# Performance work log

Hardware: AMD Instinct MI355X
Metric: run time of the kernel (lower is better)

Reference implementation:

```python
import jax, jax.numpy as jnp
import numpy as np

B, T, R = 64, 256, 256          # batch, timepoints, n_rois (T==R required by bmm path)
H, NH, DH, FF, LAT, L = 256, 8, 32, 512, 64, 2
EPS = 1e-5


def layernorm(x, g, b):
    m = x.mean(-1, keepdims=True)
    v = ((x - m) ** 2).mean(-1, keepdims=True)
    return (x - m) / jnp.sqrt(v + EPS) * g + b


def leaky_relu(x):
    return jnp.where(x >= 0, x, 0.1 * x)


def setup_inputs() -> dict:
    key = jax.random.key(0)
    ks = iter(jax.random.split(key, 64))
    def nrm(shape, s=0.02):
        return jax.random.normal(next(ks), shape, jnp.float32) * s
    return {
        "x": jax.random.normal(next(ks), (B, T, R), jnp.float32),
        "node_view": jax.random.normal(next(ks), (B, R, R), jnp.float32) * 0.1,
        "edge_view": jax.random.normal(next(ks), (B, R, R), jnp.float32) * 0.1,
        "fp_w": nrm((H, R)), "fp_b": jnp.zeros((H,)),
        "fp_g": jnp.ones((H,)), "fp_beta": jnp.zeros((H,)),
        "qkv_w": nrm((L, 3 * H, H)), "qkv_b": jnp.zeros((L, 3 * H)),
        "attn_out_w": nrm((L, H, H)), "attn_out_b": jnp.zeros((L, H)),
        "ln1_g": jnp.ones((L, H)), "ln1_b": jnp.zeros((L, H)),
        "ff1_w": nrm((L, FF, H)), "ff1_b": jnp.zeros((L, FF)),
        "ff2_w": nrm((L, H, FF)), "ff2_b": jnp.zeros((L, H)),
        "ln2_g": jnp.ones((L, H)), "ln2_b": jnp.zeros((L, H)),
        "out_w": nrm((R, H)), "out_b": jnp.zeros((R,)),
        "mu_w1": nrm((H // 2, H)), "mu_b1": jnp.zeros((H // 2,)),
        "mu_g": jnp.ones((H // 2,)), "mu_beta": jnp.zeros((H // 2,)),
        "mu_w2": nrm((LAT, H // 2)), "mu_b2": jnp.zeros((LAT,)),
        "lv_w1": nrm((H // 2, H)), "lv_b1": jnp.zeros((H // 2,)),
        "lv_g": jnp.ones((H // 2,)), "lv_beta": jnp.zeros((H // 2,)),
        "lv_w2": nrm((LAT, H // 2)), "lv_b2": jnp.zeros((LAT,)),
    }


def reference(x, node_view, edge_view, fp_w, fp_b, fp_g, fp_beta,
              qkv_w, qkv_b, attn_out_w, attn_out_b, ln1_g, ln1_b,
              ff1_w, ff1_b, ff2_w, ff2_b, ln2_g, ln2_b,
              out_w, out_b, mu_w1, mu_b1, mu_g, mu_beta, mu_w2, mu_b2,
              lv_w1, lv_b1, lv_g, lv_beta, lv_w2, lv_b2):
    # graph-view message passing: bmm(x^T, view), averaged, transposed back
    xr = jnp.swapaxes(x, 1, 2)                           # [B,R,T]
    msg = 0.5 * (jnp.einsum('brt,btq->brq', xr, node_view)
                 + jnp.einsum('brt,btq->brq', xr, edge_view))
    h = jnp.swapaxes(msg, 1, 2)                          # [B,T,R]
    # feature_proj: Linear -> LayerNorm -> LeakyReLU(0.1) -> Dropout(eval)
    h = leaky_relu(layernorm(h @ fp_w.T + fp_b, fp_g, fp_beta))  # [B,T,H]
    # TransformerEncoder (post-norm, relu FFN, dropout=identity)
    scale = 1.0 / jnp.sqrt(jnp.float32(DH))
    for i in range(L):
        qkv = h @ qkv_w[i].T + qkv_b[i]                  # [B,T,3H]
        q, k, v = jnp.split(qkv, 3, axis=-1)
        q = q.reshape(B, T, NH, DH).transpose(0, 2, 1, 3)
        k = k.reshape(B, T, NH, DH).transpose(0, 2, 1, 3)
        v = v.reshape(B, T, NH, DH).transpose(0, 2, 1, 3)
        attn = jax.nn.softmax(jnp.einsum('bhqd,bhkd->bhqk', q, k) * scale, axis=-1)
        o = jnp.einsum('bhqk,bhkd->bhqd', attn, v).transpose(0, 2, 1, 3).reshape(B, T, H)
        o = o @ attn_out_w[i].T + attn_out_b[i]
        h = layernorm(h + o, ln1_g[i], ln1_b[i])
        f = jax.nn.relu(h @ ff1_w[i].T + ff1_b[i]) @ ff2_w[i].T + ff2_b[i]
        h = layernorm(h + f, ln2_g[i], ln2_b[i])
    # fresh linear (treated as fixed params) then batched Pearson correlation
    y = h @ out_w.T + out_b                              # [B,T,R]
    data = jnp.swapaxes(y, 1, 2)                         # [B,R,T]
    c = data - data.mean(-1, keepdims=True)
    std = jnp.sqrt((c ** 2).sum(-1, keepdims=True) / (T - 1))   # unbiased, like torch.std
    cn = c / (std + 1e-8)
    corr = jnp.einsum('brt,bst->brs', cn, cn) / (T - 1)
    corr = jnp.nan_to_num(jnp.clip(corr, -1.0, 1.0), nan=0.0)   # [B,R,R]
    # heads
    pooled = h.mean(axis=1)                              # [B,H]
    mu = leaky_relu(layernorm(pooled @ mu_w1.T + mu_b1, mu_g, mu_beta)) @ mu_w2.T + mu_b2
    logvar = leaky_relu(layernorm(pooled @ lv_w1.T + lv_b1, lv_g, lv_beta)) @ lv_w2.T + lv_b2
    return mu, logvar, corr
```

## Files before the change

kernel.cpp:

```cpp
#include <hip/hip_runtime.h>
#include <hip/hip_bf16.h>
#include <math.h>

#define BB 64
#define NLAYER 2

typedef __attribute__((ext_vector_type(8))) short bfrag;
typedef __attribute__((ext_vector_type(4))) float f4_t;

__device__ __forceinline__ float dot4(float4 a, float4 b, float acc) {
    acc = fmaf(a.x, b.x, acc);
    acc = fmaf(a.y, b.y, acc);
    acc = fmaf(a.z, b.z, acc);
    acc = fmaf(a.w, b.w, acc);
    return acc;
}

__device__ __forceinline__ ushort f2bf(float f) {
    uint32_t u = __float_as_uint(f);
    uint32_t r = (u + 0x7FFFu + ((u >> 16) & 1u)) >> 16;
    return (ushort)r;
}
__device__ __forceinline__ float bf2f(ushort u) {
    return __uint_as_float(((uint32_t)u) << 16);
}

__global__ __launch_bounds__(256) void k_cvt(
    const float* __restrict__ fp_w, const float* __restrict__ qkv_w,
    const float* __restrict__ aow, const float* __restrict__ f1w,
    const float* __restrict__ f2w, const float* __restrict__ outw,
    ushort* __restrict__ dst) {
    const int g = blockIdx.x;
    const size_t idx = (size_t)g * 2048 + threadIdx.x * 8;
    const float* src;
    size_t base;
    if (g < 32)       { src = fp_w;  base = 0; }
    else if (g < 224) { src = qkv_w; base = 65536; }
    else if (g < 288) { src = aow;   base = 458752; }
    else if (g < 416) { src = f1w;   base = 589824; }
    else if (g < 544) { src = f2w;   base = 851968; }
    else              { src = outw;  base = 1114112; }
    const float4* s4 = reinterpret_cast<const float4*>(src + (idx - base));
    float4 a = s4[0], b = s4[1];
    bfrag o;
    o[0] = (short)f2bf(a.x); o[1] = (short)f2bf(a.y);
    o[2] = (short)f2bf(a.z); o[3] = (short)f2bf(a.w);
    o[4] = (short)f2bf(b.x); o[5] = (short)f2bf(b.y);
    o[6] = (short)f2bf(b.z); o[7] = (short)f2bf(b.w);
    *reinterpret_cast<bfrag*>(dst + idx) = o;
}

template <int EPI, bool WF32, bool WBF>
__global__ __launch_bounds__(256) void k_mm(
    const ushort* __restrict__ A, const ushort* __restrict__ B,
    const float* __restrict__ bias, float* __restrict__ C,
    ushort* __restrict__ Cb, int K, int N,
    size_t aStr, size_t bStr, size_t cStr) {
    __shared__ __align__(16) ushort As[128 * 72];
    __shared__ __align__(16) ushort Bs[128 * 72];
    const int tid = threadIdx.x;
    const int m0 = blockIdx.x * 128, n0 = blockIdx.y * 128;
    const size_t z = blockIdx.z;
    const int w = tid >> 6, lane = tid & 63;
    const int wm = w >> 1, wn = w & 1;
    const int fr = lane & 15, fq = lane >> 4;

    const int srow = tid >> 1, skc = (tid & 1) * 32;
    const ushort* aS = A + z * aStr + (size_t)(m0 + srow) * K + skc;
    const ushort* bS = B + z * bStr + (size_t)(n0 + srow) * K + skc;
    ushort* aD = &As[srow * 72 + skc];
    ushort* bD = &Bs[srow * 72 + skc];

    f4_t acc[4][4];
#pragma unroll
    for (int i = 0; i < 4; ++i)
#pragma unroll
        for (int j = 0; j < 4; ++j) acc[i][j] = (f4_t)0.f;

    for (int k0 = 0; k0 < K; k0 += 64) {
        {
            const bfrag* ap = reinterpret_cast<const bfrag*>(aS + k0);
            bfrag a0 = ap[0], a1 = ap[1], a2 = ap[2], a3 = ap[3];
            const bfrag* bp = reinterpret_cast<const bfrag*>(bS + k0);
            bfrag b0 = bp[0], b1 = bp[1], b2 = bp[2], b3 = bp[3];
            reinterpret_cast<bfrag*>(aD)[0] = a0;
            reinterpret_cast<bfrag*>(aD)[1] = a1;
            reinterpret_cast<bfrag*>(aD)[2] = a2;
            reinterpret_cast<bfrag*>(aD)[3] = a3;
            reinterpret_cast<bfrag*>(bD)[0] = b0;
            reinterpret_cast<bfrag*>(bD)[1] = b1;
            reinterpret_cast<bfrag*>(bD)[2] = b2;
            reinterpret_cast<bfrag*>(bD)[3] = b3;
        }
        __syncthreads();
#pragma unroll
        for (int ks = 0; ks < 2; ++ks) {
            const int kb = ks * 32 + fq * 8;
            bfrag af[4], bf[4];
#pragma unroll
            for (int fm = 0; fm < 4; ++fm)
                af[fm] = *reinterpret_cast<const bfrag*>(
                    &As[(wm * 64 + fm * 16 + fr) * 72 + kb]);
#pragma unroll
            for (int fn = 0; fn < 4; ++fn)
                bf[fn] = *reinterpret_cast<const bfrag*>(
                    &Bs[(wn * 64 + fn * 16 + fr) * 72 + kb]);
#pragma unroll
            for (int fm = 0; fm < 4; ++fm)
#pragma unroll
                for (int fn = 0; fn < 4; ++fn)
                    acc[fm][fn] = __builtin_amdgcn_mfma_f32_16x16x32_bf16(
                        bf[fn], af[fm], acc[fm][fn], 0, 0, 0);
        }
        __syncthreads();
    }

#pragma unroll
    for (int fn = 0; fn < 4; ++fn) {
        const int col0 = n0 + wn * 64 + fn * 16 + fq * 4;
        float4 bv = make_float4(0.f, 0.f, 0.f, 0.f);
        if (EPI != 3 && bias != nullptr)
            bv = *reinterpret_cast<const float4*>(&bias[col0]);
#pragma unroll
        for (int fm = 0; fm < 4; ++fm) {
            const int row = m0 + wm * 64 + fm * 16 + fr;
            float v0 = acc[fm][fn][0] + bv.x;
            float v1 = acc[fm][fn][1] + bv.y;
            float v2 = acc[fm][fn][2] + bv.z;
            float v3 = acc[fm][fn][3] + bv.w;
            if (EPI == 2) {
                v0 = fmaxf(v0, 0.f); v1 = fmaxf(v1, 0.f);
                v2 = fmaxf(v2, 0.f); v3 = fmaxf(v3, 0.f);
            }
            if (EPI == 3) {
                v0 = acc[fm][fn][0] * (1.f / 255.f);
                v1 = acc[fm][fn][1] * (1.f / 255.f);
                v2 = acc[fm][fn][2] * (1.f / 255.f);
                v3 = acc[fm][fn][3] * (1.f / 255.f);
                if (v0 != v0) v0 = 0.f;
                if (v1 != v1) v1 = 0.f;
                if (v2 != v2) v2 = 0.f;
                if (v3 != v3) v3 = 0.f;
                v0 = fminf(1.f, fmaxf(-1.f, v0));
                v1 = fminf(1.f, fmaxf(-1.f, v1));
                v2 = fminf(1.f, fmaxf(-1.f, v2));
                v3 = fminf(1.f, fmaxf(-1.f, v3));
            }
            const size_t o = cStr * z + (size_t)row * N + col0;
            if (WF32) {
                float4 fv = {v0, v1, v2, v3};
                *reinterpret_cast<float4*>(&C[o]) = fv;
            }
            if (WBF) {
                ushort4 uv;
                uv.x = f2bf(v0); uv.y = f2bf(v1);
                uv.z = f2bf(v2); uv.w = f2bf(v3);
                *reinterpret_cast<ushort4*>(&Cb[o]) = uv;
            }
        }
    }
}

template <int ACT, bool RES>
__global__ __launch_bounds__(256) void k_mmln(
    const ushort* __restrict__ A, const ushort* __restrict__ W,
    const float* __restrict__ bias, const ushort* __restrict__ res,
    const float* __restrict__ g, const float* __restrict__ bt,
    ushort* __restrict__ outb, int K) {
    __shared__ __align__(16) ushort As[32 * 72];
    __shared__ __align__(16) ushort Bs[256 * 72];
    __shared__ float redS[32][4];
    __shared__ float redQ[32][4];
    const int tid = threadIdx.x;
    const int m0 = blockIdx.x * 32;
    const int w = tid >> 6, lane = tid & 63;
    const int fr = lane & 15, fq = lane >> 4;

    const int arow = tid >> 3, akc = (tid & 7) * 8;
    const ushort* aS = A + (size_t)(m0 + arow) * K + akc;
    ushort* aD = &As[arow * 72 + akc];
    const int brow = tid >> 1, bkc = (tid & 1) * 32;
    const ushort* bS0 = W + (size_t)brow * K + bkc;
    const ushort* bS1 = W + (size_t)(brow + 128) * K + bkc;
    ushort* bD0 = &Bs[brow * 72 + bkc];
    ushort* bD1 = &Bs[(brow + 128) * 72 + bkc];

    f4_t acc[2][4];
#pragma unroll
    for (int i = 0; i < 2; ++i)
#pragma unroll
        for (int j = 0; j < 4; ++j) acc[i][j] = (f4_t)0.f;

    for (int k0 = 0; k0 < K; k0 += 64) {
        {
            bfrag a0 = *reinterpret_cast<const bfrag*>(aS + k0);
            const bfrag* bp0 = reinterpret_cast<const bfrag*>(bS0 + k0);
            bfrag b0 = bp0[0], b1 = bp0[1], b2 = bp0[2], b3 = bp0[3];
            const bfrag* bp1 = reinterpret_cast<const bfrag*>(bS1 + k0);
            bfrag c0 = bp1[0], c1 = bp1[1], c2 = bp1[2], c3 = bp1[3];
            *reinterpret_cast<bfrag*>(aD) = a0;
            reinterpret_cast<bfrag*>(bD0)[0] = b0;
            reinterpret_cast<bfrag*>(bD0)[1] = b1;
            reinterpret_cast<bfrag*>(bD0)[2] = b2;
            reinterpret_cast<bfrag*>(bD0)[3] = b3;
            reinterpret_cast<bfrag*>(bD1)[0] = c0;
            reinterpret_cast<bfrag*>(bD1)[1] = c1;
            reinterpret_cast<bfrag*>(bD1)[2] = c2;
            reinterpret_cast<bfrag*>(bD1)[3] = c3;
        }
        __syncthreads();
#pragma unroll
        for (int ks = 0; ks < 2; ++ks) {
            const int kb = ks * 32 + fq * 8;
            bfrag af[2], bf[4];
#pragma unroll
            for (int fm = 0; fm < 2; ++fm)
                af[fm] = *reinterpret_cast<const bfrag*>(
                    &As[(fm * 16 + fr) * 72 + kb]);
#pragma unroll
            for (int fn = 0; fn < 4; ++fn)
                bf[fn] = *reinterpret_cast<const bfrag*>(
                    &Bs[(w * 64 + fn * 16 + fr) * 72 + kb]);
#pragma unroll
            for (int fm = 0; fm < 2; ++fm)
#pragma unroll
                for (int fn = 0; fn < 4; ++fn)
                    acc[fm][fn] = __builtin_amdgcn_mfma_f32_16x16x32_bf16(
                        bf[fn], af[fm], acc[fm][fn], 0, 0, 0);
        }
        __syncthreads();
    }

#pragma unroll
    for (int fn = 0; fn < 4; ++fn) {
        const int col0 = w * 64 + fn * 16 + fq * 4;
        const float4 bv = *reinterpret_cast<const float4*>(&bias[col0]);
#pragma unroll
        for (int fm = 0; fm < 2; ++fm) {
            const int row = fm * 16 + fr;
            float r0 = 0.f, r1 = 0.f, r2 = 0.f, r3 = 0.f;
            if (RES) {
                ushort4 r4 = *reinterpret_cast<const ushort4*>(
                    &res[(size_t)(m0 + row) * 256 + col0]);
                r0 = bf2f(r4.x); r1 = bf2f(r4.y);
                r2 = bf2f(r4.z); r3 = bf2f(r4.w);
            }
            acc[fm][fn][0] += bv.x + r0;
            acc[fm][fn][1] += bv.y + r1;
            acc[fm][fn][2] += bv.z + r2;
            acc[fm][fn][3] += bv.w + r3;
        }
    }
#pragma unroll
    for (int fm = 0; fm < 2; ++fm) {
        float s = 0.f, q = 0.f;
#pragma unroll
        for (int fn = 0; fn < 4; ++fn)
#pragma unroll
            for (int j = 0; j < 4; ++j) {
                const float v = acc[fm][fn][j];
                s += v;
                q += v * v;
            }
        s += __shfl_xor(s, 16); q += __shfl_xor(q, 16);
        s += __shfl_xor(s, 32); q += __shfl_xor(q, 32);
        if (fq == 0) {
            redS[fm * 16 + fr][w] = s;
            redQ[fm * 16 + fr][w] = q;
        }
    }
    __syncthreads();
#pragma unroll
    for (int fm = 0; fm < 2; ++fm) {
        const int row = fm * 16 + fr;
        const float S = redS[row][0] + redS[row][1] + redS[row][2] + redS[row][3];
        const float Q = redQ[row][0] + redQ[row][1] + redQ[row][2] + redQ[row][3];
        const float mean = S * (1.f / 256.f);
        const float var = Q * (1.f / 256.f) - mean * mean;
        const float rstd = rsqrtf(fmaxf(var, 0.f) + 1e-5f);
        const size_t rowoff = (size_t)(m0 + row) * 256;
#pragma unroll
        for (int fn = 0; fn < 4; ++fn) {
            const int col0 = w * 64 + fn * 16 + fq * 4;
            const float4 g4 = *reinterpret_cast<const float4*>(&g[col0]);
            const float4 b4 = *reinterpret_cast<const float4*>(&bt[col0]);
            float v0 = (acc[fm][fn][0] - mean) * rstd * g4.x + b4.x;
            float v1 = (acc[fm][fn][1] - mean) * rstd * g4.y + b4.y;
            float v2 = (acc[fm][fn][2] - mean) * rstd * g4.z + b4.z;
            float v3 = (acc[fm][fn][3] - mean) * rstd * g4.w + b4.w;
            if (ACT == 1) {
                v0 = v0 >= 0.f ? v0 : 0.1f * v0;
                v1 = v1 >= 0.f ? v1 : 0.1f * v1;
                v2 = v2 >= 0.f ? v2 : 0.1f * v2;
                v3 = v3 >= 0.f ? v3 : 0.1f * v3;
            }
            ushort4 uv;
            uv.x = f2bf(v0); uv.y = f2bf(v1);
            uv.z = f2bf(v2); uv.w = f2bf(v3);
            *reinterpret_cast<ushort4*>(&outb[rowoff + col0]) = uv;
        }
    }
}

__global__ __launch_bounds__(256) void k_attn2(const ushort* __restrict__ qkv,
                                               ushort* __restrict__ o) {
    const int h = blockIdx.x, b = blockIdx.y;
    const int tid = threadIdx.x;
    const int w = tid >> 6, lane = tid & 63;
    const int fr = lane & 15, fq = lane >> 4;

    __shared__ __align__(16) ushort Ks[256][40];
    __shared__ __align__(16) ushort Vt[32][264];
    __shared__ __align__(16) ushort Ps[4][64][40];

    const ushort* base = qkv + (size_t)b * 196608 + h * 32;

    {
        const bfrag* kp = reinterpret_cast<const bfrag*>(base + (size_t)tid * 768 + 256);
        bfrag k0 = kp[0], k1 = kp[1], k2 = kp[2], k3 = kp[3];
        *reinterpret_cast<bfrag*>(&Ks[tid][0]) = k0;
        *reinterpret_cast<bfrag*>(&Ks[tid][8]) = k1;
        *reinterpret_cast<bfrag*>(&Ks[tid][16]) = k2;
        *reinterpret_cast<bfrag*>(&Ks[tid][24]) = k3;
    }
    {
        const bfrag* vp = reinterpret_cast<const bfrag*>(base + (size_t)tid * 768 + 512);
        bfrag v0 = vp[0], v1 = vp[1], v2 = vp[2], v3 = vp[3];
#pragma unroll
        for (int e = 0; e < 8; ++e) {
            Vt[e][tid] = (ushort)v0[e];
            Vt[8 + e][tid] = (ushort)v1[e];
            Vt[16 + e][tid] = (ushort)v2[e];
            Vt[24 + e][tid] = (ushort)v3[e];
        }
    }
    const int q0 = w * 64;
    bfrag qf[4];
#pragma unroll
    for (int fm = 0; fm < 4; ++fm)
        qf[fm] = *reinterpret_cast<const bfrag*>(
            base + (size_t)(q0 + fm * 16 + fr) * 768 + fq * 8);
    __syncthreads();

    f4_t oacc[4][2];
    float rs[4][4];
#pragma unroll
    for (int fm = 0; fm < 4; ++fm) {
        oacc[fm][0] = (f4_t)0.f;
        oacc[fm][1] = (f4_t)0.f;
#pragma unroll
        for (int j = 0; j < 4; ++j) rs[fm][j] = 0.f;
    }
    const f4_t zero4 = (f4_t)0.f;
    const float qsl = 0.17677669529663687f * 1.4426950408889634f;

    for (int kt = 0; kt < 8; ++kt) {
        bfrag kf0 = *reinterpret_cast<const bfrag*>(&Ks[kt * 32 + fr][fq * 8]);
        bfrag kf1 = *reinterpret_cast<const bfrag*>(&Ks[kt * 32 + 16 + fr][fq * 8]);
        f4_t s0[4], s1[4];
#pragma unroll
        for (int fm = 0; fm < 4; ++fm) {
            s0[fm] = __builtin_amdgcn_mfma_f32_16x16x32_bf16(qf[fm], kf0, zero4, 0, 0, 0);
            s1[fm] = __builtin_amdgcn_mfma_f32_16x16x32_bf16(qf[fm], kf1, zero4, 0, 0, 0);
        }
#pragma unroll
        for (int fm = 0; fm < 4; ++fm) {
#pragma unroll
            for (int j = 0; j < 4; ++j) {
                const int row = fm * 16 + fq * 4 + j;
                ushort u0 = f2bf(exp2f(s0[fm][j] * qsl));
                ushort u1 = f2bf(exp2f(s1[fm][j] * qsl));
                Ps[w][row][fr] = u0;
                Ps[w][row][16 + fr] = u1;
                rs[fm][j] += bf2f(u0) + bf2f(u1);
            }
        }
        bfrag vf0 = *reinterpret_cast<const bfrag*>(&Vt[fr][kt * 32 + fq * 8]);
        bfrag vf1 = *reinterpret_cast<const bfrag*>(&Vt[16 + fr][kt * 32 + fq * 8]);
        bfrag pf[4];
#pragma unroll
        for (int fm = 0; fm < 4; ++fm)
            pf[fm] = *reinterpret_cast<const bfrag*>(&Ps[w][fm * 16 + fr][fq * 8]);
#pragma unroll
        for (int fm = 0; fm < 4; ++fm) {
            oacc[fm][0] = __builtin_amdgcn_mfma_f32_16x16x32_bf16(pf[fm], vf0, oacc[fm][0], 0, 0, 0);
            oacc[fm][1] = __builtin_amdgcn_mfma_f32_16x16x32_bf16(pf[fm], vf1, oacc[fm][1], 0, 0, 0);
        }
    }

#pragma unroll
    for (int fm = 0; fm < 4; ++fm)
#pragma unroll
        for (int j = 0; j < 4; ++j) {
            float r = rs[fm][j];
            r += __shfl_xor(r, 1);
            r += __shfl_xor(r, 2);
            r += __shfl_xor(r, 4);
            r += __shfl_xor(r, 8);
            rs[fm][j] = 1.f / r;
        }
    ushort* ob = o + (size_t)b * 65536 + h * 32;
#pragma unroll
    for (int fm = 0; fm < 4; ++fm) {
        const int qrow = q0 + fm * 16 + fq * 4;
#pragma unroll
        for (int j = 0; j < 4; ++j) {
            const float inv = rs[fm][j];
            ob[(size_t)(qrow + j) * 256 + fr] = f2bf(oacc[fm][0][j] * inv);
            ob[(size_t)(qrow + j) * 256 + 16 + fr] = f2bf(oacc[fm][1][j] * inv);
        }
    }
}

__global__ __launch_bounds__(256) void k_xpose_bmm(
    const float* __restrict__ x, const float* __restrict__ nv,
    const float* __restrict__ ev, ushort* __restrict__ At,
    ushort* __restrict__ Xt) {
    const int b = blockIdx.z;
    const int k0 = blockIdx.x * 64, i0 = blockIdx.y * 64;
    __shared__ float TA[64][65];
    __shared__ float TX[64][65];
    const size_t bb = (size_t)b * 65536;
    const int tid = threadIdx.x;
    const int lr = tid >> 4, lc = (tid & 15) * 4;
#pragma unroll
    for (int l = 0; l < 4; ++l) {
        const int row = lr + l * 16;
        const size_t gidx = bb + (size_t)(k0 + row) * 256 + i0 + lc;
        float4 n4 = *reinterpret_cast<const float4*>(nv + gidx);
        float4 e4 = *reinterpret_cast<const float4*>(ev + gidx);
        float4 x4 = *reinterpret_cast<const float4*>(x + gidx);
        TA[row][lc] = 0.5f * (n4.x + e4.x);
        TA[row][lc + 1] = 0.5f * (n4.y + e4.y);
        TA[row][lc + 2] = 0.5f * (n4.z + e4.z);
        TA[row][lc + 3] = 0.5f * (n4.w + e4.w);
        TX[row][lc] = x4.x;
        TX[row][lc + 1] = x4.y;
        TX[row][lc + 2] = x4.z;
        TX[row][lc + 3] = x4.w;
    }
    __syncthreads();
    const int i = tid & 63, kk = (tid >> 6) * 16;
    bfrag a0, a1, x0, x1;
#pragma unroll
    for (int e = 0; e < 8; ++e) {
        a0[e] = (short)f2bf(TA[kk + e][i]);
        a1[e] = (short)f2bf(TA[kk + 8 + e][i]);
        x0[e] = (short)f2bf(TX[kk + e][i]);
        x1[e] = (short)f2bf(TX[kk + 8 + e][i]);
    }
    const size_t o = bb + (size_t)(i0 + i) * 256 + k0 + kk;
    *reinterpret_cast<bfrag*>(At + o) = a0;
    *reinterpret_cast<bfrag*>(At + o + 8) = a1;
    *reinterpret_cast<bfrag*>(Xt + o) = x0;
    *reinterpret_cast<bfrag*>(Xt + o + 8) = x1;
}

__global__ __launch_bounds__(256) void k_colstats2(const ushort* __restrict__ y,
                                                   float* __restrict__ stats) {
    const int b = blockIdx.y, rq = blockIdx.x;
    const int rl = threadIdx.x & 63, tc = threadIdx.x >> 6;
    const int r = rq * 64 + rl;
    const ushort* yb = y + (size_t)b * 65536 + (size_t)tc * 64 * 256;
    float s = 0.f, q = 0.f;
    for (int t = 0; t < 64; ++t) {
        float v = bf2f(yb[t * 256 + r]);
        s += v;
        q += v * v;
    }
    __shared__ float ps[4][64];
    __shared__ float pq[4][64];
    ps[tc][rl] = s;
    pq[tc][rl] = q;
    __syncthreads();
    if (tc == 0) {
        float S = ps[0][rl] + ps[1][rl] + ps[2][rl] + ps[3][rl];
        float Q = pq[0][rl] + pq[1][rl] + pq[2][rl] + pq[3][rl];
        const float mean = S * (1.f / 256.f);
        const float var = (Q - S * mean) * (1.f / 255.f);
        const float stdv = sqrtf(fmaxf(var, 0.f));
        stats[b * 512 + r] = mean;
        stats[b * 512 + 256 + r] = 1.f / (stdv + 1e-8f);
    }
}

__global__ __launch_bounds__(256) void k_xpose_cn(
    const ushort* __restrict__ y, const float* __restrict__ stats,
    ushort* __restrict__ cnT) {
    const int b = blockIdx.z;
    const int t0 = blockIdx.x * 64, r0 = blockIdx.y * 64;
    __shared__ float T[64][65];
    const size_t bb = (size_t)b * 65536;
    const int tid = threadIdx.x;
    const int lr = tid >> 4, lc = (tid & 15) * 4;
#pragma unroll
    for (int l = 0; l < 4; ++l) {
        const int row = lr + l * 16;
        const size_t gidx = bb + (size_t)(t0 + row) * 256 + r0 + lc;
        ushort4 y4 = *reinterpret_cast<const ushort4*>(y + gidx);
        T[row][lc] = bf2f(y4.x);
        T[row][lc + 1] = bf2f(y4.y);
        T[row][lc + 2] = bf2f(y4.z);
        T[row][lc + 3] = bf2f(y4.w);
    }
    __syncthreads();
    const int i = tid & 63, kk = (tid >> 6) * 16;
    const float mean = stats[b * 512 + r0 + i];
    const float inv = stats[b * 512 + 256 + r0 + i];
    bfrag c0, c1;
#pragma unroll
    for (int e = 0; e < 8; ++e) {
        c0[e] = (short)f2bf((T[kk + e][i] - mean) * inv);
        c1[e] = (short)f2bf((T[kk + 8 + e][i] - mean) * inv);
    }
    const size_t o = bb + (size_t)(r0 + i) * 256 + t0 + kk;
    *reinterpret_cast<bfrag*>(cnT + o) = c0;
    *reinterpret_cast<bfrag*>(cnT + o + 8) = c1;
}

__global__ __launch_bounds__(1024) void k_pool(const ushort* __restrict__ h,
                                               float* __restrict__ pooled) {
    const int b = blockIdx.x;
    const int c = threadIdx.x & 255, tc = threadIdx.x >> 8;
    const ushort* hb = h + (size_t)b * 65536 + (size_t)tc * 64 * 256;
    float s = 0.f;
    for (int t = 0; t < 64; ++t) s += bf2f(hb[t * 256 + c]);
    __shared__ float pp[4][256];
    pp[tc][c] = s;
    __syncthreads();
    if (tc == 0)
        pooled[b * 256 + c] = (pp[0][c] + pp[1][c] + pp[2][c] + pp[3][c]) * (1.f / 256.f);
}

__global__ __launch_bounds__(128) void k_head(
    const float* __restrict__ pooled,
    const float* __restrict__ mw1, const float* __restrict__ mb1,
    const float* __restrict__ mg, const float* __restrict__ mbt,
    const float* __restrict__ mw2, const float* __restrict__ mb2,
    const float* __restrict__ lw1, const float* __restrict__ lb1,
    const float* __restrict__ lg, const float* __restrict__ lbt,
    const float* __restrict__ lw2, const float* __restrict__ lb2,
    float* __restrict__ outp) {
    const int b = blockIdx.x, hd = blockIdx.y;
    const int tid = threadIdx.x;
    const float* w1 = hd ? lw1 : mw1;
    const float* b1 = hd ? lb1 : mb1;
    const float* g = hd ? lg : mg;
    const float* bt = hd ? lbt : mbt;
    const float* w2 = hd ? lw2 : mw2;
    const float* b2 = hd ? lb2 : mb2;

    __shared__ float pl[256];
    __shared__ float t1[128];
    __shared__ float redS[2];
    __shared__ float redQ[2];

    pl[tid] = pooled[b * 256 + tid];
    pl[tid + 128] = pooled[b * 256 + tid + 128];
    __syncthreads();

    float a = b1[tid];
    const float4* w1v = (const float4*)(w1 + (size_t)tid * 256);
#pragma unroll 4
    for (int k4 = 0; k4 < 64; ++k4) {
        float4 w = w1v[k4];
        float4 p = *(const float4*)&pl[k4 * 4];
        a = dot4(p, w, a);
    }
    float s = a, q = a * a;
#pragma unroll
    for (int m = 1; m < 64; m <<= 1) {
        s += __shfl_xor(s, m);
        q += __shfl_xor(q, m);
    }
    if ((tid & 63) == 0) { redS[tid >> 6] = s; redQ[tid >> 6] = q; }
    __syncthreads();
    const float mean = (redS[0] + redS[1]) * (1.f / 128.f);
    const float var = (redQ[0] + redQ[1]) * (1.f / 128.f) - mean * mean;
    const float rstd = rsqrtf(fmaxf(var, 0.f) + 1e-5f);
    float v = (a - mean) * rstd * g[tid] + bt[tid];
    v = v >= 0.f ? v : 0.1f * v;
    t1[tid] = v;
    __syncthreads();
    if (tid < 64) {
        float o = b2[tid];
        const float* w2r = w2 + (size_t)tid * 128;
#pragma unroll 4
        for (int c = 0; c < 128; ++c) o = fmaf(t1[c], w2r[c], o);
        outp[hd * 4096 + b * 64 + tid] = o;
    }
}

extern "C" void kernel_launch(void* const* d_in, const int* in_sizes, int n_in,
                              void* d_out, int out_size, void* d_ws, size_t ws_size,
                              hipStream_t stream) {
    const float* x = (const float*)d_in[0];
    const float* nv = (const float*)d_in[1];
    const float* ev = (const float*)d_in[2];
    const float* fp_w = (const float*)d_in[3];
    const float* fp_b = (const float*)d_in[4];
    const float* fp_g = (const float*)d_in[5];
    const float* fp_beta = (const float*)d_in[6];
    const float* qkv_w = (const float*)d_in[7];
    const float* qkv_b = (const float*)d_in[8];
    const float* aow = (const float*)d_in[9];
    const float* aob = (const float*)d_in[10];
    const float* ln1g = (const float*)d_in[11];
    const float* ln1b = (const float*)d_in[12];
    const float* f1w = (const float*)d_in[13];
    const float* f1b = (const float*)d_in[14];
    const float* f2w = (const float*)d_in[15];
    const float* f2b = (const float*)d_in[16];
    const float* ln2g = (const float*)d_in[17];
    const float* ln2b = (const float*)d_in[18];
    const float* outw = (const float*)d_in[19];
    const float* outb = (const float*)d_in[20];
    const float* muw1 = (const float*)d_in[21];
    const float* mub1 = (const float*)d_in[22];
    const float* mug = (const float*)d_in[23];
    const float* mubt = (const float*)d_in[24];
    const float* muw2 = (const float*)d_in[25];
    const float* mub2 = (const float*)d_in[26];
    const float* lvw1 = (const float*)d_in[27];
    const float* lvb1 = (const float*)d_in[28];
    const float* lvg = (const float*)d_in[29];
    const float* lvbt = (const float*)d_in[30];
    const float* lvw2 = (const float*)d_in[31];
    const float* lvb2 = (const float*)d_in[32];

    float* out = (float*)d_out;
    float* ws = (float*)d_ws;

    float* stats = ws;
    float* pooled = ws + 32768;
    ushort* ub = (ushort*)(ws + 65536);
    ushort* wh_bf = ub;
    ushort* qkvb = ub + 4194304;
    ushort* At = qkvb;
    ushort* Xt = qkvb + 4194304;
    ushort* o_bf = ub + 16777216;
    ushort* h0_bf = o_bf;
    ushort* f1_bf = ub + 20971520;
    ushort* cnT = f1_bf;
    ushort* y_bf = ub + 29360128;
    ushort* wbf = ub + 33554432;

    k_cvt<<<576, 256, 0, stream>>>(fp_w, qkv_w, aow, f1w, f2w, outw, wbf);

    k_xpose_bmm<<<dim3(4, 4, BB), 256, 0, stream>>>(x, nv, ev, At, Xt);
    k_mm<0, false, true><<<dim3(2, 2, BB), 256, 0, stream>>>(
        At, Xt, nullptr, nullptr, h0_bf, 256, 256, 65536, 65536, 65536);

    k_mmln<1, false><<<512, 256, 0, stream>>>(
        h0_bf, wbf, fp_b, nullptr, fp_g, fp_beta, wh_bf, 256);

    for (int l = 0; l < NLAYER; ++l) {
        k_mm<0, false, true><<<dim3(128, 6, 1), 256, 0, stream>>>(
            wh_bf, wbf + 65536 + (size_t)l * 196608, qkv_b + l * 768,
            nullptr, qkvb, 256, 768, 0, 0, 0);
        k_attn2<<<dim3(8, BB), 256, 0, stream>>>(qkvb, o_bf);
        k_mmln<0, true><<<512, 256, 0, stream>>>(
            o_bf, wbf + 458752 + (size_t)l * 65536, aob + l * 256,
            wh_bf, ln1g + l * 256, ln1b + l * 256, wh_bf, 256);
        k_mm<2, false, true><<<dim3(128, 4, 1), 256, 0, stream>>>(
            wh_bf, wbf + 589824 + (size_t)l * 131072, f1b + l * 512,
            nullptr, f1_bf, 256, 512, 0, 0, 0);
        k_mmln<0, true><<<512, 256, 0, stream>>>(
            f1_bf, wbf + 851968 + (size_t)l * 131072, f2b + l * 256,
            wh_bf, ln2g + l * 256, ln2b + l * 256, wh_bf, 512);
    }

    k_mm<0, false, true><<<dim3(128, 2, 1), 256, 0, stream>>>(
        wh_bf, wbf + 1114112, outb, nullptr, y_bf, 256, 256, 0, 0, 0);

    k_colstats2<<<dim3(4, BB), 256, 0, stream>>>(y_bf, stats);
    k_xpose_cn<<<dim3(4, 4, BB), 256, 0, stream>>>(y_bf, stats, cnT);
    k_mm<3, true, false><<<dim3(2, 2, BB), 256, 0, stream>>>(
        cnT, cnT, nullptr, out + 8192, nullptr, 256, 256, 65536, 65536, 65536);

    k_pool<<<BB, 1024, 0, stream>>>(wh_bf, pooled);
    k_head<<<dim3(BB, 2), 128, 0, stream>>>(
        pooled, muw1, mub1, mug, mubt, muw2, mub2,
        lvw1, lvb1, lvg, lvbt, lvw2, lvb2, out);
}
```

Before: 254.1 us.

## Prefetch GEMM tiles into registers, halve M tile, fuse column stats into transpose

Both GEMM kernels now load the next K-slice from global memory into registers before the current slice's MFMA work, so load latency overlaps compute. The generic k_mm tile shrinks from 128x128 to 64x128, doubling grid sizes for better CU occupancy on these small GEMMs. The Pearson column-stats and normalize-transpose kernels are merged into a single k_pstats kernel, dropping one launch and the stats round trip through global memory. In exchange there is more register pressure and less reuse per tile.

New measurement: 252.3 us. No clear change (-0.7%).

```diff
diff --git a/kernel.cpp b/kernel.cpp
--- a/kernel.cpp
+++ b/kernel.cpp
@@ -56,57 +56,64 @@
     const float* __restrict__ bias, float* __restrict__ C,
     ushort* __restrict__ Cb, int K, int N,
     size_t aStr, size_t bStr, size_t cStr) {
-    __shared__ __align__(16) ushort As[128 * 72];
+    __shared__ __align__(16) ushort As[64 * 72];
     __shared__ __align__(16) ushort Bs[128 * 72];
     const int tid = threadIdx.x;
-    const int m0 = blockIdx.x * 128, n0 = blockIdx.y * 128;
+    const int m0 = blockIdx.x * 64, n0 = blockIdx.y * 128;
     const size_t z = blockIdx.z;
     const int w = tid >> 6, lane = tid & 63;
     const int wm = w >> 1, wn = w & 1;
     const int fr = lane & 15, fq = lane >> 4;
 
-    const int srow = tid >> 1, skc = (tid & 1) * 32;
-    const ushort* aS = A + z * aStr + (size_t)(m0 + srow) * K + skc;
-    const ushort* bS = B + z * bStr + (size_t)(n0 + srow) * K + skc;
-    ushort* aD = &As[srow * 72 + skc];
-    ushort* bD = &Bs[srow * 72 + skc];
-
-    f4_t acc[4][4];
-#pragma unroll
-    for (int i = 0; i < 4; ++i)
+    const int arow = tid >> 2, akc = (tid & 3) * 16;
+    const ushort* aS = A + z * aStr + (size_t)(m0 + arow) * K + akc;
+    ushort* aD = &As[arow * 72 + akc];
+    const int brow = tid >> 1, bkc = (tid & 1) * 32;
+    const ushort* bS = B + z * bStr + (size_t)(n0 + brow) * K + bkc;
+    ushort* bD = &Bs[brow * 72 + bkc];
+
+    f4_t acc[2][4];
+#pragma unroll
+    for (int i = 0; i < 2; ++i)
 #pragma unroll
         for (int j = 0; j < 4; ++j) acc[i][j] = (f4_t)0.f;
 
+    bfrag ra0, ra1, rb0, rb1, rb2, rb3;
+    {
+        const bfrag* ap = reinterpret_cast<const bfrag*>(aS);
+        ra0 = ap[0]; ra1 = ap[1];
+        const bfrag* bp = reinterpret_cast<const bfrag*>(bS);
+        rb0 = bp[0]; rb1 = bp[1]; rb2 = bp[2]; rb3 = bp[3];
+    }
+
     for (int k0 = 0; k0 < K; k0 += 64) {
-        {
-            const bfrag* ap = reinterpret_cast<const bfrag*>(aS + k0);
-            bfrag a0 = ap[0], a1 = ap[1], a2 = ap[2], a3 = ap[3];
-            const bfrag* bp = reinterpret_cast<const bfrag*>(bS + k0);
-            bfrag b0 = bp[0], b1 = bp[1], b2 = bp[2], b3 = bp[3];
-            reinterpret_cast<bfrag*>(aD)[0] = a0;
-            reinterpret_cast<bfrag*>(aD)[1] = a1;
-            reinterpret_cast<bfrag*>(aD)[2] = a2;
-            reinterpret_cast<bfrag*>(aD)[3] = a3;
-            reinterpret_cast<bfrag*>(bD)[0] = b0;
-            reinterpret_cast<bfrag*>(bD)[1] = b1;
-            reinterpret_cast<bfrag*>(bD)[2] = b2;
-            reinterpret_cast<bfrag*>(bD)[3] = b3;
-        }
+        reinterpret_cast<bfrag*>(aD)[0] = ra0;
+        reinterpret_cast<bfrag*>(aD)[1] = ra1;
+        reinterpret_cast<bfrag*>(bD)[0] = rb0;
+        reinterpret_cast<bfrag*>(bD)[1] = rb1;
+        reinterpret_cast<bfrag*>(bD)[2] = rb2;
+        reinterpret_cast<bfrag*>(bD)[3] = rb3;
         __syncthreads();
+        if (k0 + 64 < K) {
+            const bfrag* ap = reinterpret_cast<const bfrag*>(aS + k0 + 64);
+            ra0 = ap[0]; ra1 = ap[1];
+            const bfrag* bp = reinterpret_cast<const bfrag*>(bS + k0 + 64);
+            rb0 = bp[0]; rb1 = bp[1]; rb2 = bp[2]; rb3 = bp[3];
+        }
 #pragma unroll
         for (int ks = 0; ks < 2; ++ks) {
             const int kb = ks * 32 + fq * 8;
-            bfrag af[4], bf[4];
-#pragma unroll
-            for (int fm = 0; fm < 4; ++fm)
+            bfrag af[2], bf[4];
+#pragma unroll
+            for (int fm = 0; fm < 2; ++fm)
                 af[fm] = *reinterpret_cast<const bfrag*>(
-                    &As[(wm * 64 + fm * 16 + fr) * 72 + kb]);
+                    &As[(wm * 32 + fm * 16 + fr) * 72 + kb]);
 #pragma unroll
             for (int fn = 0; fn < 4; ++fn)
                 bf[fn] = *reinterpret_cast<const bfrag*>(
                     &Bs[(wn * 64 + fn * 16 + fr) * 72 + kb]);
 #pragma unroll
-            for (int fm = 0; fm < 4; ++fm)
+            for (int fm = 0; fm < 2; ++fm)
 #pragma unroll
                 for (int fn = 0; fn < 4; ++fn)
                     acc[fm][fn] = __builtin_amdgcn_mfma_f32_16x16x32_bf16(
@@ -122,8 +129,8 @@
         if (EPI != 3 && bias != nullptr)
             bv = *reinterpret_cast<const float4*>(&bias[col0]);
 #pragma unroll
-        for (int fm = 0; fm < 4; ++fm) {
-            const int row = m0 + wm * 64 + fm * 16 + fr;
+        for (int fm = 0; fm < 2; ++fm) {
+            const int row = m0 + wm * 32 + fm * 16 + fr;
             float v0 = acc[fm][fn][0] + bv.x;
             float v1 = acc[fm][fn][1] + bv.y;
             float v2 = acc[fm][fn][2] + bv.z;
@@ -191,24 +198,33 @@
 #pragma unroll
         for (int j = 0; j < 4; ++j) acc[i][j] = (f4_t)0.f;
 
+    bfrag ra, rb0, rb1, rb2, rb3, rc0, rc1, rc2, rc3;
+    {
+        ra = *reinterpret_cast<const bfrag*>(aS);
+        const bfrag* bp0 = reinterpret_cast<const bfrag*>(bS0);
+        rb0 = bp0[0]; rb1 = bp0[1]; rb2 = bp0[2]; rb3 = bp0[3];
+        const bfrag* bp1 = reinterpret_cast<const bfrag*>(bS1);
+        rc0 = bp1[0]; rc1 = bp1[1]; rc2 = bp1[2]; rc3 = bp1[3];
+    }
+
     for (int k0 = 0; k0 < K; k0 += 64) {
-        {
-            bfrag a0 = *reinterpret_cast<const bfrag*>(aS + k0);
-            const bfrag* bp0 = reinterpret_cast<const bfrag*>(bS0 + k0);
-            bfrag b0 = bp0[0], b1 = bp0[1], b2 = bp0[2], b3 = bp0[3];
-            const bfrag* bp1 = reinterpret_cast<const bfrag*>(bS1 + k0);
-            bfrag c0 = bp1[0], c1 = bp1[1], c2 = bp1[2], c3 = bp1[3];
-            *reinterpret_cast<bfrag*>(aD) = a0;
-            reinterpret_cast<bfrag*>(bD0)[0] = b0;
-            reinterpret_cast<bfrag*>(bD0)[1] = b1;
-            reinterpret_cast<bfrag*>(bD0)[2] = b2;
-            reinterpret_cast<bfrag*>(bD0)[3] = b3;
-            reinterpret_cast<bfrag*>(bD1)[0] = c0;
-            reinterpret_cast<bfrag*>(bD1)[1] = c1;
-            reinterpret_cast<bfrag*>(bD1)[2] = c2;
-            reinterpret_cast<bfrag*>(bD1)[3] = c3;
-        }
+        *reinterpret_cast<bfrag*>(aD) = ra;
+        reinterpret_cast<bfrag*>(bD0)[0] = rb0;
+        reinterpret_cast<bfrag*>(bD0)[1] = rb1;
+        reinterpret_cast<bfrag*>(bD0)[2] = rb2;
+        reinterpret_cast<bfrag*>(bD0)[3] = rb3;
+        reinterpret_cast<bfrag*>(bD1)[0] = rc0;
+        reinterpret_cast<bfrag*>(bD1)[1] = rc1;
+        reinterpret_cast<bfrag*>(bD1)[2] = rc2;
+        reinterpret_cast<bfrag*>(bD1)[3] = rc3;
         __syncthreads();
+        if (k0 + 64 < K) {
+            ra = *reinterpret_cast<const bfrag*>(aS + k0 + 64);
+            const bfrag* bp0 = reinterpret_cast<const bfrag*>(bS0 + k0 + 64);
+            rb0 = bp0[0]; rb1 = bp0[1]; rb2 = bp0[2]; rb3 = bp0[3];
+            const bfrag* bp1 = reinterpret_cast<const bfrag*>(bS1 + k0 + 64);
+            rc0 = bp1[0]; rc1 = bp1[1]; rc2 = bp1[2]; rc3 = bp1[3];
+        }
 #pragma unroll
         for (int ks = 0; ks < 2; ++ks) {
             const int kb = ks * 32 + fq * 8;
@@ -456,66 +472,55 @@
     *reinterpret_cast<bfrag*>(Xt + o + 8) = x1;
 }
 
-__global__ __launch_bounds__(256) void k_colstats2(const ushort* __restrict__ y,
-                                                   float* __restrict__ stats) {
-    const int b = blockIdx.y, rq = blockIdx.x;
-    const int rl = threadIdx.x & 63, tc = threadIdx.x >> 6;
-    const int r = rq * 64 + rl;
-    const ushort* yb = y + (size_t)b * 65536 + (size_t)tc * 64 * 256;
-    float s = 0.f, q = 0.f;
-    for (int t = 0; t < 64; ++t) {
-        float v = bf2f(yb[t * 256 + r]);
-        s += v;
-        q += v * v;
-    }
-    __shared__ float ps[4][64];
-    __shared__ float pq[4][64];
-    ps[tc][rl] = s;
-    pq[tc][rl] = q;
-    __syncthreads();
-    if (tc == 0) {
-        float S = ps[0][rl] + ps[1][rl] + ps[2][rl] + ps[3][rl];
-        float Q = pq[0][rl] + pq[1][rl] + pq[2][rl] + pq[3][rl];
+__global__ __launch_bounds__(256) void k_pstats(const ushort* __restrict__ y,
+                                                ushort* __restrict__ cnT) {
+    const int b = blockIdx.y, r0 = blockIdx.x * 64;
+    __shared__ __align__(16) ushort T[256][72];
+    __shared__ float sred[4][64];
+    __shared__ float qred[4][64];
+    __shared__ float mstat[64];
+    __shared__ float istat[64];
+    const int tid = threadIdx.x;
+    {
+        const bfrag* yv = reinterpret_cast<const bfrag*>(
+            y + (size_t)b * 65536 + (size_t)tid * 256 + r0);
+#pragma unroll
+        for (int i = 0; i < 8; ++i)
+            *reinterpret_cast<bfrag*>(&T[tid][i * 8]) = yv[i];
+    }
+    __syncthreads();
+    const int rl = tid & 63, tc = tid >> 6;
+    {
+        float s = 0.f, q = 0.f;
+        for (int t = 0; t < 64; ++t) {
+            float v = bf2f(T[tc * 64 + t][rl]);
+            s += v;
+            q += v * v;
+        }
+        sred[tc][rl] = s;
+        qred[tc][rl] = q;
+    }
+    __syncthreads();
+    if (tid < 64) {
+        const float S = sred[0][tid] + sred[1][tid] + sred[2][tid] + sred[3][tid];
+        const float Q = qred[0][tid] + qred[1][tid] + qred[2][tid] + qred[3][tid];
         const float mean = S * (1.f / 256.f);
         const float var = (Q - S * mean) * (1.f / 255.f);
         const float stdv = sqrtf(fmaxf(var, 0.f));
-        stats[b * 512 + r] = mean;
-        stats[b * 512 + 256 + r] = 1.f / (stdv + 1e-8f);
-    }
-}
-
-__global__ __launch_bounds__(256) void k_xpose_cn(
-    const ushort* __restrict__ y, const float* __restrict__ stats,
-    ushort* __restrict__ cnT) {
-    const int b = blockIdx.z;
-    const int t0 = blockIdx.x * 64, r0 = blockIdx.y * 64;
-    __shared__ float T[64][65];
-    const size_t bb = (size_t)b * 65536;
-    const int tid = threadIdx.x;
-    const int lr = tid >> 4, lc = (tid & 15) * 4;
-#pragma unroll
-    for (int l = 0; l < 4; ++l) {
-        const int row = lr + l * 16;
-        const size_t gidx = bb + (size_t)(t0 + row) * 256 + r0 + lc;
-        ushort4 y4 = *reinterpret_cast<const ushort4*>(y + gidx);
-        T[row][lc] = bf2f(y4.x);
-        T[row][lc + 1] = bf2f(y4.y);
-        T[row][lc + 2] = bf2f(y4.z);
-        T[row][lc + 3] = bf2f(y4.w);
-    }
-    __syncthreads();
-    const int i = tid & 63, kk = (tid >> 6) * 16;
-    const float mean = stats[b * 512 + r0 + i];
-    const float inv = stats[b * 512 + 256 + r0 + i];
-    bfrag c0, c1;
-#pragma unroll
-    for (int e = 0; e < 8; ++e) {
-        c0[e] = (short)f2bf((T[kk + e][i] - mean) * inv);
-        c1[e] = (short)f2bf((T[kk + 8 + e][i] - mean) * inv);
-    }
-    const size_t o = bb + (size_t)(r0 + i) * 256 + t0 + kk;
-    *reinterpret_cast<bfrag*>(cnT + o) = c0;
-    *reinterpret_cast<bfrag*>(cnT + o + 8) = c1;
+        mstat[tid] = mean;
+        istat[tid] = 1.f / (stdv + 1e-8f);
+    }
+    __syncthreads();
+    const float mean = mstat[rl], inv = istat[rl];
+    ushort* dst = cnT + (size_t)b * 65536 + (size_t)(r0 + rl) * 256 + tc * 64;
+#pragma unroll
+    for (int i = 0; i < 8; ++i) {
+        bfrag c;
+#pragma unroll
+        for (int e = 0; e < 8; ++e)
+            c[e] = (short)f2bf((bf2f(T[tc * 64 + i * 8 + e][rl]) - mean) * inv);
+        reinterpret_cast<bfrag*>(dst)[i] = c;
+    }
 }
 
 __global__ __launch_bounds__(1024) void k_pool(const ushort* __restrict__ h,
@@ -631,9 +636,8 @@
     float* out = (float*)d_out;
     float* ws = (float*)d_ws;
 
-    float* stats = ws;
-    float* pooled = ws + 32768;
-    ushort* ub = (ushort*)(ws + 65536);
+    float* pooled = ws;
+    ushort* ub = (ushort*)(ws + 32768);
     ushort* wh_bf = ub;
     ushort* qkvb = ub + 4194304;
     ushort* At = qkvb;
@@ -648,21 +652,21 @@
     k_cvt<<<576, 256, 0, stream>>>(fp_w, qkv_w, aow, f1w, f2w, outw, wbf);
 
     k_xpose_bmm<<<dim3(4, 4, BB), 256, 0, stream>>>(x, nv, ev, At, Xt);
-    k_mm<0, false, true><<<dim3(2, 2, BB), 256, 0, stream>>>(
+    k_mm<0, false, true><<<dim3(4, 2, BB), 256, 0, stream>>>(
         At, Xt, nullptr, nullptr, h0_bf, 256, 256, 65536, 65536, 65536);
 
     k_mmln<1, false><<<512, 256, 0, stream>>>(
         h0_bf, wbf, fp_b, nullptr, fp_g, fp_beta, wh_bf, 256);
 
     for (int l = 0; l < NLAYER; ++l) {
-        k_mm<0, false, true><<<dim3(128, 6, 1), 256, 0, stream>>>(
+        k_mm<0, false, true><<<dim3(256, 6, 1), 256, 0, stream>>>(
             wh_bf, wbf + 65536 + (size_t)l * 196608, qkv_b + l * 768,
             nullptr, qkvb, 256, 768, 0, 0, 0);
         k_attn2<<<dim3(8, BB), 256, 0, stream>>>(qkvb, o_bf);
         k_mmln<0, true><<<512, 256, 0, stream>>>(
             o_bf, wbf + 458752 + (size_t)l * 65536, aob + l * 256,
             wh_bf, ln1g + l * 256, ln1b + l * 256, wh_bf, 256);
-        k_mm<2, false, true><<<dim3(128, 4, 1), 256, 0, stream>>>(
+        k_mm<2, false, true><<<dim3(256, 4, 1), 256, 0, stream>>>(
             wh_bf, wbf + 589824 + (size_t)l * 131072, f1b + l * 512,
             nullptr, f1_bf, 256, 512, 0, 0, 0);
         k_mmln<0, true><<<512, 256, 0, stream>>>(
@@ -670,12 +674,11 @@
             wh_bf, ln2g + l * 256, ln2b + l * 256, wh_bf, 512);
     }
 
-    k_mm<0, false, true><<<dim3(128, 2, 1), 256, 0, stream>>>(
+    k_mm<0, false, true><<<dim3(256, 2, 1), 256, 0, stream>>>(
         wh_bf, wbf + 1114112, outb, nullptr, y_bf, 256, 256, 0, 0, 0);
 
-    k_colstats2<<<dim3(4, BB), 256, 0, stream>>>(y_bf, stats);
-    k_xpose_cn<<<dim3(4, 4, BB), 256, 0, stream>>>(y_bf, stats, cnT);
-    k_mm<3, true, false><<<dim3(2, 2, BB), 256, 0, stream>>>(
+    k_pstats<<<dim3(4, BB), 256, 0, stream>>>(y_bf, cnT);
+    k_mm<3, true, false><<<dim3(4, 2, BB), 256, 0, stream>>>(
         cnT, cnT, nullptr, out + 8192, nullptr, 256, 256, 65536, 65536, 65536);
 
     k_pool<<<BB, 1024, 0, stream>>>(wh_bf, pooled);
```
